# Optimization experiments

Hardware: AMD Instinct MI355X
Metric: run time of the kernel (lower is better)

The kernel has to match this reference:

```python
import jax, jax.numpy as jnp
import numpy as np

H = 512   # hidden_size
B = 32    # batch
S = 2048  # src_len
NEG = -1e10


def setup_inputs() -> dict:
    key = jax.random.key(0)
    k1, k2, k3, k4, k5, k6 = jax.random.split(key, 6)
    hidden = jax.random.normal(k1, (B, 2 * H), dtype=jnp.float32)
    encoder_outputs = jax.random.normal(k2, (S, B, 2 * H), dtype=jnp.float32)
    mask = jax.random.randint(k3, (B, S), 0, 2, dtype=jnp.int32)
    # params: nn.Linear(4H, H) -> weight [H, 4H], bias [H]; v ~ U[0,1) [H]
    bound = 1.0 / np.sqrt(4 * H)
    attn_w = jax.random.uniform(k4, (H, 4 * H), minval=-bound, maxval=bound, dtype=jnp.float32)
    attn_b = jax.random.uniform(k5, (H,), minval=-bound, maxval=bound, dtype=jnp.float32)
    v = jax.random.uniform(k6, (H,), dtype=jnp.float32)
    return {"hidden": hidden, "encoder_outputs": encoder_outputs, "mask": mask,
            "attn_w": attn_w, "attn_b": attn_b, "v": v}


def reference(hidden, encoder_outputs, mask, attn_w, attn_b, v):
    # hidden: [B, 2H] -> [B, S, 2H]; encoder_outputs: [S, B, 2H] -> [B, S, 2H]
    src_len = encoder_outputs.shape[0]
    h = jnp.broadcast_to(hidden[:, None, :], (hidden.shape[0], src_len, hidden.shape[1]))
    eo = jnp.transpose(encoder_outputs, (1, 0, 2))
    cat = jnp.concatenate((h, eo), axis=2)                      # [B, S, 4H]
    energy = jnp.tanh(jnp.einsum('bsf,hf->bsh', cat, attn_w) + attn_b)  # [B, S, H]
    attention = jnp.einsum('bsh,h->bs', energy, v)              # [B, S]
    attention = jnp.where(mask == 0, NEG, attention)
    return jax.nn.softmax(attention, axis=1)
```

## Files before the change

### kernel.cpp

```cpp
#include <hip/hip_runtime.h>

#define SLEN 2048
#define BATCH 32
#define HDIM 512
#define KDIM 1024

typedef _Float16 f16x8 __attribute__((ext_vector_type(8)));
typedef _Float16 f16x4 __attribute__((ext_vector_type(4)));
typedef float f32x4 __attribute__((ext_vector_type(4)));

__device__ __forceinline__ void gload16(const void* g, void* l) {
  __builtin_amdgcn_global_load_lds(
      (const __attribute__((address_space(1))) unsigned int*)g,
      (__attribute__((address_space(3))) unsigned int*)l, 16, 0, 0);
}

__device__ __forceinline__ float fast_tanh(float x) {
  float e = __expf(2.0f * x);
  return 1.0f - 2.0f * __builtin_amdgcn_rcpf(e + 1.0f);
}

__global__ __launch_bounds__(256) void prep_k(const float* __restrict__ attn_w,
                                              const float* __restrict__ attn_b,
                                              const float* __restrict__ hidden,
                                              const float* __restrict__ eo,
                                              _Float16* __restrict__ Bt,
                                              float* __restrict__ s1,
                                              float* __restrict__ score,
                                              _Float16* __restrict__ eo16) {
  if (blockIdx.x < 512) {
    int t = blockIdx.x * 256 + threadIdx.x;
    int h = t >> 8;
    int c = t & 255;
    float4 x = *(const float4*)(attn_w + (size_t)h * 2048 + 1024 + c * 4);
    f16x4 y = {(_Float16)x.x, (_Float16)x.y, (_Float16)x.z, (_Float16)x.w};
    *(f16x4*)(Bt + (size_t)h * 1024 + c * 4) = y;
  } else if (blockIdx.x < 4608) {
    int o = (blockIdx.x - 512) * 4 + (threadIdx.x >> 6);
    int b = o >> 9, h = o & 511;
    int lane = threadIdx.x & 63;
    const float4* hp = (const float4*)(hidden + (size_t)b * 1024);
    const float4* wp = (const float4*)(attn_w + (size_t)h * 2048);
    float acc = 0.f;
#pragma unroll
    for (int c = 0; c < 4; ++c) {
      float4 a = hp[c * 64 + lane];
      float4 wv = wp[c * 64 + lane];
      acc += a.x * wv.x + a.y * wv.y + a.z * wv.z + a.w * wv.w;
    }
#pragma unroll
    for (int off = 1; off < 64; off <<= 1) acc += __shfl_xor(acc, off);
    if (lane == 0) s1[o] = acc + attn_b[h];
  } else if (blockIdx.x < 4640) {
    int idx = (blockIdx.x - 4608) * 256 + threadIdx.x;
    float4 z = {0.f, 0.f, 0.f, 0.f};
    ((float4*)score)[idx] = z;
    ((float4*)score)[idx + 8192] = z;
  } else {
    int g = (blockIdx.x - 4640) * 256 + threadIdx.x;
    const float4* src = (const float4*)eo;
#pragma unroll
    for (int it = 0; it < 16; ++it) {
      size_t c = (size_t)it * 524288 + g;
      float4 a = src[c * 2];
      float4 b2 = src[c * 2 + 1];
      f16x8 o = {(_Float16)a.x,  (_Float16)a.y,  (_Float16)a.z,  (_Float16)a.w,
                 (_Float16)b2.x, (_Float16)b2.y, (_Float16)b2.z, (_Float16)b2.w};
      *(f16x8*)(eo16 + c * 8) = o;
    }
  }
}

__global__ __launch_bounds__(256, 3) void gemm_k(const _Float16* __restrict__ eo16,
                                                 const _Float16* __restrict__ Bt,
                                                 const float* __restrict__ s1,
                                                 const float* __restrict__ v,
                                                 float* __restrict__ score) {
  constexpr int BK = 32;
  constexpr int NKT = KDIM / BK;
  __shared__ __align__(16) char smem[49152];

  int bid = blockIdx.x;
  int x = bid & 7;
  int q = bid >> 3;
  int nt = q & 3;
  int mt = (q >> 2) * 8 + x;

  int tid = threadIdx.x;
  int lane = tid & 63;
  int w = tid >> 6;
  int wm = (w >> 1) * 64;
  int wn = (w & 1) * 64;

  const _Float16* ga[2];
  const _Float16* gb[2];
  int swz = ((lane & 3) ^ ((lane >> 3) & 3)) << 3;
#pragma unroll
  for (int i = 0; i < 2; ++i) {
    ga[i] = eo16 + (size_t)(mt * 128 + 32 * w + 16 * i + (lane >> 2)) * KDIM + swz;
    gb[i] = Bt + (size_t)(nt * 128 + 32 * w + 16 * i + (lane >> 2)) * KDIM + swz;
  }

  f32x4 acc[4][4];
#pragma unroll
  for (int i = 0; i < 4; ++i)
#pragma unroll
    for (int j = 0; j < 4; ++j) acc[i][j] = (f32x4){0.f, 0.f, 0.f, 0.f};

  int mrow = lane & 15;
  int quad = lane >> 4;
  int rc = (quad ^ ((mrow >> 1) & 3)) << 3;

#define STAGE(buf)                                                    \
  {                                                                   \
    gload16(ga[0], smem + (buf)*8192 + (w * 2 + 0) * 1024);           \
    gload16(ga[1], smem + (buf)*8192 + (w * 2 + 1) * 1024);           \
    ga[0] += BK; ga[1] += BK;                                         \
    gload16(gb[0], smem + 24576 + (buf)*8192 + (w * 2 + 0) * 1024);   \
    gload16(gb[1], smem + 24576 + (buf)*8192 + (w * 2 + 1) * 1024);   \
    gb[0] += BK; gb[1] += BK;                                         \
  }

  STAGE(0);
  STAGE(1);

  int cur = 0, nx2 = 2;
  for (int kt = 0; kt < NKT; ++kt) {
    if (kt + 2 < NKT) {
      STAGE(nx2);
      asm volatile("s_waitcnt vmcnt(8)" ::: "memory");
    } else if (kt + 1 < NKT) {
      asm volatile("s_waitcnt vmcnt(4)" ::: "memory");
    } else {
      asm volatile("s_waitcnt vmcnt(0)" ::: "memory");
    }
    __builtin_amdgcn_s_barrier();

    const _Float16* Ab = (const _Float16*)(smem + cur * 8192);
    const _Float16* Bb = (const _Float16*)(smem + 24576 + cur * 8192);
    f16x8 af[4], bf[4];
#pragma unroll
    for (int i = 0; i < 4; ++i)
      af[i] = *(const f16x8*)&Ab[(wm + 16 * i + mrow) * BK + rc];
#pragma unroll
    for (int j = 0; j < 4; ++j)
      bf[j] = *(const f16x8*)&Bb[(wn + 16 * j + mrow) * BK + rc];

    asm volatile("s_waitcnt lgkmcnt(0)" ::: "memory");
    __builtin_amdgcn_sched_barrier(0);
    __builtin_amdgcn_s_barrier();

    __builtin_amdgcn_s_setprio(1);
#pragma unroll
    for (int i = 0; i < 4; ++i)
#pragma unroll
      for (int j = 0; j < 4; ++j)
        acc[i][j] = __builtin_amdgcn_mfma_f32_16x16x32_f16(af[i], bf[j], acc[i][j], 0, 0, 0);
    __builtin_amdgcn_s_setprio(0);

    cur = (cur == 2) ? 0 : cur + 1;
    nx2 = (nx2 == 2) ? 0 : nx2 + 1;
  }
#undef STAGE

  __syncthreads();
  float* s1s = (float*)smem;
  float* vsm = (float*)(smem + 48640);
  for (int t = tid; t < 1024; t += 256) {
    int bb = t >> 5, cc = t & 31;
    ((float4*)s1s)[bb * 33 + cc] = *(const float4*)(s1 + (size_t)bb * 512 + nt * 128 + cc * 4);
  }
  if (tid < 32) ((float4*)vsm)[tid] = *(const float4*)(v + nt * 128 + tid * 4);
  __syncthreads();

  int lcol = mrow;
  float vv[4];
#pragma unroll
  for (int j = 0; j < 4; ++j) vv[j] = vsm[wn + 16 * j + lcol];

#pragma unroll
  for (int i = 0; i < 4; ++i) {
#pragma unroll
    for (int r = 0; r < 4; ++r) {
      int mloc = wm + 16 * i + 4 * quad + r;
      int bb = mloc & 31;
      float sum = 0.f;
#pragma unroll
      for (int j = 0; j < 4; ++j) {
        float e = acc[i][j][r] + s1s[bb * 132 + wn + 16 * j + lcol];
        sum += fast_tanh(e) * vv[j];
      }
      sum += __shfl_xor(sum, 1);
      sum += __shfl_xor(sum, 2);
      sum += __shfl_xor(sum, 4);
      sum += __shfl_xor(sum, 8);
      if (lcol == 0) {
        int mg = mt * 128 + mloc;
        atomicAdd(&score[(mg & 31) * SLEN + (mg >> 5)], sum);
      }
    }
  }
}

__global__ __launch_bounds__(256) void softmax_k(const float* __restrict__ score,
                                                 const int* __restrict__ mask,
                                                 float* __restrict__ out) {
  int b = blockIdx.x;
  int tid = threadIdx.x;
  int lane = tid & 63, w = tid >> 6;
  __shared__ float red[8];
  float vals[8];
  float mx = -3.4e38f;
#pragma unroll
  for (int i = 0; i < 8; ++i) {
    int s = i * 256 + tid;
    float xv = score[b * SLEN + s];
    if (mask[b * SLEN + s] == 0) xv = -1e10f;
    vals[i] = xv;
    mx = fmaxf(mx, xv);
  }
#pragma unroll
  for (int off = 1; off < 64; off <<= 1) mx = fmaxf(mx, __shfl_xor(mx, off));
  if (lane == 0) red[w] = mx;
  __syncthreads();
  mx = fmaxf(fmaxf(red[0], red[1]), fmaxf(red[2], red[3]));
  float sum = 0.f;
#pragma unroll
  for (int i = 0; i < 8; ++i) {
    vals[i] = __expf(vals[i] - mx);
    sum += vals[i];
  }
#pragma unroll
  for (int off = 1; off < 64; off <<= 1) sum += __shfl_xor(sum, off);
  if (lane == 0) red[4 + w] = sum;
  __syncthreads();
  sum = red[4] + red[5] + red[6] + red[7];
  float inv = 1.0f / sum;
#pragma unroll
  for (int i = 0; i < 8; ++i) out[b * SLEN + i * 256 + tid] = vals[i] * inv;
}

extern "C" void kernel_launch(void* const* d_in, const int* in_sizes, int n_in,
                              void* d_out, int out_size, void* d_ws, size_t ws_size,
                              hipStream_t stream) {
  const float* hidden = (const float*)d_in[0];
  const float* eo     = (const float*)d_in[1];
  const int*   mask   = (const int*)d_in[2];
  const float* attn_w = (const float*)d_in[3];
  const float* attn_b = (const float*)d_in[4];
  const float* v      = (const float*)d_in[5];
  float* out = (float*)d_out;

  char* wsb = (char*)d_ws;
  _Float16* Bt = (_Float16*)wsb;
  float* s1    = (float*)(wsb + (1 << 20));
  float* score = (float*)(wsb + (1 << 20) + (1 << 16));
  _Float16* eo16 = (_Float16*)(wsb + (2 << 20));

  prep_k<<<6688, 256, 0, stream>>>(attn_w, attn_b, hidden, eo, Bt, s1, score, eo16);
  gemm_k<<<2048, 256, 0, stream>>>(eo16, Bt, s1, v, score);
  softmax_k<<<BATCH, 256, 0, stream>>>(score, mask, out);
}
```

Measured before the change: 518.1 us.

## Fuse fp32-to-fp16 conversion of encoder outputs into GEMM register-staged loads

Removes the separate pass that converted the fp32 encoder outputs to fp16 in workspace. The GEMM now reads fp32 directly into registers, converts it there, and writes padded fp16 tiles into double-buffered LDS. Loads for the next tiles are prefetched into registers while the current tile is consumed by MFMA. This drops a full read and write of the 128MB-scale intermediate, but the GEMM now reads fp32 A, twice the bytes of fp16, and re-reads it once per N tile (four times), and it loses the async global-to-LDS loads.

Result: faster. 484.0 us (-6.6%).

```diff
diff --git a/kernel.cpp b/kernel.cpp
--- a/kernel.cpp
+++ b/kernel.cpp
@@ -9,12 +9,6 @@
 typedef _Float16 f16x4 __attribute__((ext_vector_type(4)));
 typedef float f32x4 __attribute__((ext_vector_type(4)));
 
-__device__ __forceinline__ void gload16(const void* g, void* l) {
-  __builtin_amdgcn_global_load_lds(
-      (const __attribute__((address_space(1))) unsigned int*)g,
-      (__attribute__((address_space(3))) unsigned int*)l, 16, 0, 0);
-}
-
 __device__ __forceinline__ float fast_tanh(float x) {
   float e = __expf(2.0f * x);
   return 1.0f - 2.0f * __builtin_amdgcn_rcpf(e + 1.0f);
@@ -23,11 +17,9 @@
 __global__ __launch_bounds__(256) void prep_k(const float* __restrict__ attn_w,
                                               const float* __restrict__ attn_b,
                                               const float* __restrict__ hidden,
-                                              const float* __restrict__ eo,
                                               _Float16* __restrict__ Bt,
                                               float* __restrict__ s1,
-                                              float* __restrict__ score,
-                                              _Float16* __restrict__ eo16) {
+                                              float* __restrict__ score) {
   if (blockIdx.x < 512) {
     int t = blockIdx.x * 256 + threadIdx.x;
     int h = t >> 8;
@@ -51,34 +43,21 @@
 #pragma unroll
     for (int off = 1; off < 64; off <<= 1) acc += __shfl_xor(acc, off);
     if (lane == 0) s1[o] = acc + attn_b[h];
-  } else if (blockIdx.x < 4640) {
+  } else {
     int idx = (blockIdx.x - 4608) * 256 + threadIdx.x;
     float4 z = {0.f, 0.f, 0.f, 0.f};
     ((float4*)score)[idx] = z;
     ((float4*)score)[idx + 8192] = z;
-  } else {
-    int g = (blockIdx.x - 4640) * 256 + threadIdx.x;
-    const float4* src = (const float4*)eo;
-#pragma unroll
-    for (int it = 0; it < 16; ++it) {
-      size_t c = (size_t)it * 524288 + g;
-      float4 a = src[c * 2];
-      float4 b2 = src[c * 2 + 1];
-      f16x8 o = {(_Float16)a.x,  (_Float16)a.y,  (_Float16)a.z,  (_Float16)a.w,
-                 (_Float16)b2.x, (_Float16)b2.y, (_Float16)b2.z, (_Float16)b2.w};
-      *(f16x8*)(eo16 + c * 8) = o;
-    }
-  }
-}
-
-__global__ __launch_bounds__(256, 3) void gemm_k(const _Float16* __restrict__ eo16,
+  }
+}
+
+__global__ __launch_bounds__(256, 3) void gemm_k(const float* __restrict__ eo,
                                                  const _Float16* __restrict__ Bt,
                                                  const float* __restrict__ s1,
                                                  const float* __restrict__ v,
                                                  float* __restrict__ score) {
-  constexpr int BK = 32;
-  constexpr int NKT = KDIM / BK;
-  __shared__ __align__(16) char smem[49152];
+  constexpr int NKT = KDIM / 32;
+  __shared__ __align__(16) char smem[40960];
 
   int bid = blockIdx.x;
   int x = bid & 7;
@@ -91,81 +70,104 @@
   int w = tid >> 6;
   int wm = (w >> 1) * 64;
   int wn = (w & 1) * 64;
-
-  const _Float16* ga[2];
-  const _Float16* gb[2];
-  int swz = ((lane & 3) ^ ((lane >> 3) & 3)) << 3;
-#pragma unroll
-  for (int i = 0; i < 2; ++i) {
-    ga[i] = eo16 + (size_t)(mt * 128 + 32 * w + 16 * i + (lane >> 2)) * KDIM + swz;
-    gb[i] = Bt + (size_t)(nt * 128 + 32 * w + 16 * i + (lane >> 2)) * KDIM + swz;
-  }
-
-  f32x4 acc[4][4];
-#pragma unroll
-  for (int i = 0; i < 4; ++i)
-#pragma unroll
-    for (int j = 0; j < 4; ++j) acc[i][j] = (f32x4){0.f, 0.f, 0.f, 0.f};
-
   int mrow = lane & 15;
   int quad = lane >> 4;
-  int rc = (quad ^ ((mrow >> 1) & 3)) << 3;
-
-#define STAGE(buf)                                                    \
-  {                                                                   \
-    gload16(ga[0], smem + (buf)*8192 + (w * 2 + 0) * 1024);           \
-    gload16(ga[1], smem + (buf)*8192 + (w * 2 + 1) * 1024);           \
-    ga[0] += BK; ga[1] += BK;                                         \
-    gload16(gb[0], smem + 24576 + (buf)*8192 + (w * 2 + 0) * 1024);   \
-    gload16(gb[1], smem + 24576 + (buf)*8192 + (w * 2 + 1) * 1024);   \
-    gb[0] += BK; gb[1] += BK;                                         \
-  }
-
-  STAGE(0);
-  STAGE(1);
-
-  int cur = 0, nx2 = 2;
-  for (int kt = 0; kt < NKT; ++kt) {
-    if (kt + 2 < NKT) {
-      STAGE(nx2);
-      asm volatile("s_waitcnt vmcnt(8)" ::: "memory");
-    } else if (kt + 1 < NKT) {
-      asm volatile("s_waitcnt vmcnt(4)" ::: "memory");
-    } else {
-      asm volatile("s_waitcnt vmcnt(0)" ::: "memory");
-    }
-    __builtin_amdgcn_s_barrier();
-
-    const _Float16* Ab = (const _Float16*)(smem + cur * 8192);
-    const _Float16* Bb = (const _Float16*)(smem + 24576 + cur * 8192);
-    f16x8 af[4], bf[4];
-#pragma unroll
-    for (int i = 0; i < 4; ++i)
-      af[i] = *(const f16x8*)&Ab[(wm + 16 * i + mrow) * BK + rc];
-#pragma unroll
-    for (int j = 0; j < 4; ++j)
-      bf[j] = *(const f16x8*)&Bb[(wn + 16 * j + mrow) * BK + rc];
-
-    asm volatile("s_waitcnt lgkmcnt(0)" ::: "memory");
-    __builtin_amdgcn_sched_barrier(0);
-    __builtin_amdgcn_s_barrier();
-
-    __builtin_amdgcn_s_setprio(1);
-#pragma unroll
-    for (int i = 0; i < 4; ++i)
-#pragma unroll
-      for (int j = 0; j < 4; ++j)
-        acc[i][j] = __builtin_amdgcn_mfma_f32_16x16x32_f16(af[i], bf[j], acc[i][j], 0, 0, 0);
-    __builtin_amdgcn_s_setprio(0);
-
-    cur = (cur == 2) ? 0 : cur + 1;
-    nx2 = (nx2 == 2) ? 0 : nx2 + 1;
-  }
-#undef STAGE
+
+  const float* aBase = eo + (size_t)(mt * 128 + 32 * w + (lane >> 1)) * KDIM + (lane & 1) * 16;
+  const _Float16* bBase = Bt + (size_t)(nt * 128 + 32 * w + (lane >> 1)) * KDIM + (lane & 1) * 16;
+  int wrOff = (32 * w + (lane >> 1)) * 80 + (lane & 1) * 32;
+
+  char* sm = (char*)smem;
+
+  f32x4 acc[4][4];
+#pragma unroll
+  for (int i = 0; i < 4; ++i)
+#pragma unroll
+    for (int j = 0; j < 4; ++j) acc[i][j] = (f32x4){0.f, 0.f, 0.f, 0.f};
+
+  float4 A0a, A0b, A0c, A0d, B0a, B0b;
+  float4 A1a, A1b, A1c, A1d, B1a, B1b;
+
+#define LOADREG(Aa, Ab, Ac, Ad, Ba, Bb, T)                        \
+  {                                                               \
+    int kc = ((T) < NKT ? (T) : NKT - 1) * 32;                    \
+    Aa = *(const float4*)(aBase + kc);                            \
+    Ab = *(const float4*)(aBase + kc + 4);                        \
+    Ac = *(const float4*)(aBase + kc + 8);                        \
+    Ad = *(const float4*)(aBase + kc + 12);                       \
+    Ba = *(const float4*)(bBase + kc);                            \
+    Bb = *(const float4*)(bBase + kc + 8);                        \
+  }
+
+#define WRITEBUF(BASE, Aa, Ab, Ac, Ad, Ba, Bb)                                    \
+  {                                                                               \
+    f16x8 p0 = {(_Float16)Aa.x, (_Float16)Aa.y, (_Float16)Aa.z, (_Float16)Aa.w,  \
+                (_Float16)Ab.x, (_Float16)Ab.y, (_Float16)Ab.z, (_Float16)Ab.w}; \
+    f16x8 p1 = {(_Float16)Ac.x, (_Float16)Ac.y, (_Float16)Ac.z, (_Float16)Ac.w,  \
+                (_Float16)Ad.x, (_Float16)Ad.y, (_Float16)Ad.z, (_Float16)Ad.w}; \
+    *(f16x8*)(sm + (BASE) + wrOff) = p0;                                          \
+    *(f16x8*)(sm + (BASE) + wrOff + 16) = p1;                                     \
+    *(float4*)(sm + (BASE) + 10240 + wrOff) = Ba;                                 \
+    *(float4*)(sm + (BASE) + 10240 + wrOff + 16) = Bb;                            \
+  }
+
+#define KSTEP(CURB, OTHB, Aa, Ab, Ac, Ad, Ba, Bb, TNEXT)                          \
+  {                                                                               \
+    f16x8 af0 = *(const f16x8*)(sm + (CURB) + (wm + mrow) * 80 + quad * 16);      \
+    f16x8 af1 = *(const f16x8*)(sm + (CURB) + (wm + 16 + mrow) * 80 + quad * 16); \
+    f16x8 af2 = *(const f16x8*)(sm + (CURB) + (wm + 32 + mrow) * 80 + quad * 16); \
+    f16x8 af3 = *(const f16x8*)(sm + (CURB) + (wm + 48 + mrow) * 80 + quad * 16); \
+    f16x8 bf0 = *(const f16x8*)(sm + (CURB) + 10240 + (wn + mrow) * 80 + quad * 16);      \
+    f16x8 bf1 = *(const f16x8*)(sm + (CURB) + 10240 + (wn + 16 + mrow) * 80 + quad * 16); \
+    f16x8 bf2 = *(const f16x8*)(sm + (CURB) + 10240 + (wn + 32 + mrow) * 80 + quad * 16); \
+    f16x8 bf3 = *(const f16x8*)(sm + (CURB) + 10240 + (wn + 48 + mrow) * 80 + quad * 16); \
+    __builtin_amdgcn_s_setprio(1);                                                \
+    acc[0][0] = __builtin_amdgcn_mfma_f32_16x16x32_f16(af0, bf0, acc[0][0], 0, 0, 0); \
+    acc[0][1] = __builtin_amdgcn_mfma_f32_16x16x32_f16(af0, bf1, acc[0][1], 0, 0, 0); \
+    acc[0][2] = __builtin_amdgcn_mfma_f32_16x16x32_f16(af0, bf2, acc[0][2], 0, 0, 0); \
+    acc[0][3] = __builtin_amdgcn_mfma_f32_16x16x32_f16(af0, bf3, acc[0][3], 0, 0, 0); \
+    acc[1][0] = __builtin_amdgcn_mfma_f32_16x16x32_f16(af1, bf0, acc[1][0], 0, 0, 0); \
+    acc[1][1] = __builtin_amdgcn_mfma_f32_16x16x32_f16(af1, bf1, acc[1][1], 0, 0, 0); \
+    acc[1][2] = __builtin_amdgcn_mfma_f32_16x16x32_f16(af1, bf2, acc[1][2], 0, 0, 0); \
+    acc[1][3] = __builtin_amdgcn_mfma_f32_16x16x32_f16(af1, bf3, acc[1][3], 0, 0, 0); \
+    acc[2][0] = __builtin_amdgcn_mfma_f32_16x16x32_f16(af2, bf0, acc[2][0], 0, 0, 0); \
+    acc[2][1] = __builtin_amdgcn_mfma_f32_16x16x32_f16(af2, bf1, acc[2][1], 0, 0, 0); \
+    acc[2][2] = __builtin_amdgcn_mfma_f32_16x16x32_f16(af2, bf2, acc[2][2], 0, 0, 0); \
+    acc[2][3] = __builtin_amdgcn_mfma_f32_16x16x32_f16(af2, bf3, acc[2][3], 0, 0, 0); \
+    acc[3][0] = __builtin_amdgcn_mfma_f32_16x16x32_f16(af3, bf0, acc[3][0], 0, 0, 0); \
+    acc[3][1] = __builtin_amdgcn_mfma_f32_16x16x32_f16(af3, bf1, acc[3][1], 0, 0, 0); \
+    acc[3][2] = __builtin_amdgcn_mfma_f32_16x16x32_f16(af3, bf2, acc[3][2], 0, 0, 0); \
+    acc[3][3] = __builtin_amdgcn_mfma_f32_16x16x32_f16(af3, bf3, acc[3][3], 0, 0, 0); \
+    __builtin_amdgcn_s_setprio(0);                                                \
+    asm volatile("s_waitcnt vmcnt(6)" ::: "memory");                              \
+    WRITEBUF(OTHB, Aa, Ab, Ac, Ad, Ba, Bb);                                       \
+    LOADREG(Aa, Ab, Ac, Ad, Ba, Bb, TNEXT);                                       \
+    asm volatile("s_waitcnt lgkmcnt(0)" ::: "memory");                            \
+    __builtin_amdgcn_sched_barrier(0);                                            \
+    __builtin_amdgcn_s_barrier();                                                 \
+  }
+
+  LOADREG(A0a, A0b, A0c, A0d, B0a, B0b, 0);
+  asm volatile("s_waitcnt vmcnt(0)" ::: "memory");
+  WRITEBUF(0, A0a, A0b, A0c, A0d, B0a, B0b);
+  LOADREG(A0a, A0b, A0c, A0d, B0a, B0b, 1);
+  LOADREG(A1a, A1b, A1c, A1d, B1a, B1b, 2);
+  asm volatile("s_waitcnt lgkmcnt(0)" ::: "memory");
+  __builtin_amdgcn_sched_barrier(0);
+  __builtin_amdgcn_s_barrier();
+
+#pragma unroll 1
+  for (int it = 0; it < NKT / 2; ++it) {
+    KSTEP(0, 20480, A0a, A0b, A0c, A0d, B0a, B0b, 2 * it + 3);
+    KSTEP(20480, 0, A1a, A1b, A1c, A1d, B1a, B1b, 2 * it + 4);
+  }
+#undef KSTEP
+#undef WRITEBUF
+#undef LOADREG
 
   __syncthreads();
   float* s1s = (float*)smem;
-  float* vsm = (float*)(smem + 48640);
+  float* vsm = (float*)(smem + 16896);
   for (int t = tid; t < 1024; t += 256) {
     int bb = t >> 5, cc = t & 31;
     ((float4*)s1s)[bb * 33 + cc] = *(const float4*)(s1 + (size_t)bb * 512 + nt * 128 + cc * 4);
@@ -255,9 +257,8 @@
   _Float16* Bt = (_Float16*)wsb;
   float* s1    = (float*)(wsb + (1 << 20));
   float* score = (float*)(wsb + (1 << 20) + (1 << 16));
-  _Float16* eo16 = (_Float16*)(wsb + (2 << 20));
-
-  prep_k<<<6688, 256, 0, stream>>>(attn_w, attn_b, hidden, eo, Bt, s1, score, eo16);
-  gemm_k<<<2048, 256, 0, stream>>>(eo16, Bt, s1, v, score);
+
+  prep_k<<<4640, 256, 0, stream>>>(attn_w, attn_b, hidden, Bt, s1, score);
+  gemm_k<<<2048, 256, 0, stream>>>(eo, Bt, s1, v, score);
   softmax_k<<<BATCH, 256, 0, stream>>>(score, mask, out);
 }
```
